# Kernel tuning notes

Hardware: AMD Instinct MI355X
Metric: run time of the kernel (lower is better)

The kernel has to match this reference:

```python
import jax, jax.numpy as jnp
import numpy as np

HEADS = 8

def setup_inputs() -> dict:
    key = jax.random.key(0)
    k1, k2, k3, k4 = jax.random.split(key, 4)
    B, C_IN, H, W = 16, 256, 64, 64
    C_OUT = 256
    s = 1.0 / np.sqrt(C_IN)
    x = jax.random.normal(k1, (B, C_IN, H, W), dtype=jnp.float32)
    wq = jax.random.normal(k2, (C_OUT, C_IN), dtype=jnp.float32) * s
    wk = jax.random.normal(k3, (C_OUT, C_IN), dtype=jnp.float32) * s
    wv = jax.random.normal(k4, (C_OUT, C_IN), dtype=jnp.float32) * s
    return {"x": x, "wq": wq, "wk": wk, "wv": wv}

def _feat(t):
    # ELU(x) + 1  (positive feature map for linear attention)
    return jax.nn.elu(t) + 1.0

def reference(x, wq, wk, wv):
    B, C, H, W = x.shape
    M = H * W
    c_out = wq.shape[0]
    dh = c_out // HEADS
    scale = 1.0 / np.sqrt(dh)
    xf = x.reshape(B, C, M)  # flatten spatial
    # 1x1 conv (no bias) == channel matmul; reshape to [B, heads, dh, M]
    def proj(w):
        return jnp.einsum('oc,bcm->bom', w, xf).reshape(B, HEADS, dh, M)
    q = _feat(proj(wq)) * scale
    k = _feat(proj(wk)) * scale
    v = proj(wv)
    # linear attention: KV = k v^T over spatial, then apply to q
    KV = jnp.einsum('bhcm,bhdm->bhcd', k, v)          # [B,h,dh,dh]
    out = jnp.einsum('bhcd,bhcm->bhdm', KV, q)        # [B,h,dh,M]
    k_sum = k.sum(axis=-1)                             # [B,h,dh]
    denom = jnp.einsum('bhcm,bhc->bhm', q, k_sum)      # [B,h,M]
    denom = jnp.maximum(denom, 1e-6)[:, :, None, :]
    out = out / denom
    return out.reshape(B, c_out, H, W)
```

## Files before the change

### kernel.cpp

```cpp
#include <hip/hip_runtime.h>
#include <hip/hip_bf16.h>


typedef __attribute__((ext_vector_type(8))) short bf16x8;
typedef __attribute__((ext_vector_type(4))) float f32x4;
typedef __attribute__((ext_vector_type(4))) unsigned int u32x4;
typedef __attribute__((ext_vector_type(4))) float float4v;

#define DEVI static __device__ __forceinline__

DEVI unsigned short f2bf(float f){
  unsigned int u = __builtin_bit_cast(unsigned int, f);
  u = (u + 0x7fffu + ((u >> 16) & 1u)) >> 16;
  return (unsigned short)u;
}
DEVI unsigned int pk2(float a, float b){
  return (unsigned int)f2bf(a) | ((unsigned int)f2bf(b) << 16);
}
DEVI float feat(float p){
  return (p > 0.f ? p + 1.f : __expf(p)) * 0.17677669529663687f;
}

DEVI f32x4 mfma16(u32x4 a, u32x4 b, f32x4 c){
  return __builtin_amdgcn_mfma_f32_16x16x32_bf16(
      __builtin_bit_cast(bf16x8, a), __builtin_bit_cast(bf16x8, b), c, 0, 0, 0);
}

DEVI int swz8(int m){ return ((m ^ (m >> 3)) & 7) << 4; }

typedef __attribute__((address_space(3))) unsigned int as3_u32;
typedef __attribute__((address_space(1))) const unsigned int as1_u32;
DEVI void gload16(const void* g, void* l){
  __builtin_amdgcn_global_load_lds((as1_u32*)g, (as3_u32*)l, 16, 0, 0);
}
DEVI void stage_tile(const char* src, void* buf, int w, int lane){
  #pragma unroll
  for (int i = 0; i < 4; ++i){
    int ub = w * 1024 + i * 8192;
    gload16(src + ub + lane * 16, (char*)buf + ub);
  }
}

DEVI void stage_load(const float* __restrict__ xb, int m0, int tid, float4v* r){
  #pragma unroll
  for (int it = 0; it < 2; ++it){
    int cq = (tid >> 4) + it * 32;
    int mq = tid & 15;
    const float* p = xb + (size_t)(cq * 4) * 4096 + m0 + mq * 4;
    r[it*4+0] = *(const float4v*)(p);
    r[it*4+1] = *(const float4v*)(p + 4096);
    r[it*4+2] = *(const float4v*)(p + 8192);
    r[it*4+3] = *(const float4v*)(p + 12288);
  }
}
DEVI void stage_write(unsigned short* xT, int tid, const float4v* r){
  #pragma unroll
  for (int it = 0; it < 2; ++it){
    int cq = (tid >> 4) + it * 32;
    int mq = tid & 15;
    int c0 = cq * 4, ml0 = mq * 4;
    #pragma unroll
    for (int j = 0; j < 4; ++j){
      int m = ml0 + j;
      unsigned int lo = pk2(r[it*4+0][j], r[it*4+1][j]);
      unsigned int hi = pk2(r[it*4+2][j], r[it*4+3][j]);
      int off = m * 512 + ((c0 * 2) ^ swz8(m));
      unsigned long long v = (unsigned long long)lo | ((unsigned long long)hi << 32);
      *(unsigned long long*)((char*)xT + off) = v;
    }
  }
}

DEVI void wpack(int t, const float* __restrict__ wq, const float* __restrict__ wk,
                const float* __restrict__ wv,
                unsigned short* __restrict__ wkvf, unsigned short* __restrict__ wqf){
  if (t < 16384){
    int lane = t & 63, kk = (t >> 6) & 7, ot = (t >> 9) & 3, h = t >> 11;
    int l15 = lane & 15, hi = lane >> 4;
    const float* src = (ot < 2) ? (wk + (size_t)(h * 32 + ot * 16 + l15) * 256)
                                : (wv + (size_t)(h * 32 + (ot - 2) * 16 + l15) * 256);
    src += kk * 32 + hi * 8;
    unsigned short* dst = wkvf + (size_t)t * 8;
    #pragma unroll
    for (int j = 0; j < 8; ++j) dst[j] = f2bf(src[j]);
  } else if (t < 24576){
    int u = t - 16384;
    int lane = u & 63, kk = (u >> 6) & 7, ot = (u >> 9) & 1, h = u >> 10;
    int l15 = lane & 15, hi = lane >> 4;
    const float* src = wq + (size_t)(h * 32 + ot * 16 + l15) * 256 + kk * 32 + hi * 8;
    unsigned short* dst = wqf + (size_t)u * 8;
    #pragma unroll
    for (int j = 0; j < 8; ++j) dst[j] = f2bf(src[j]);
  }
}

__global__ void __launch_bounds__(512) xcvt(const float* __restrict__ x,
        const float* __restrict__ wq, const float* __restrict__ wk,
        const float* __restrict__ wv,
        unsigned short* __restrict__ wkvf, unsigned short* __restrict__ wqf,
        unsigned short* __restrict__ ximg){
  __shared__ __align__(16) unsigned short xT[16384];
  const int tid = threadIdx.x;
  const int ch = blockIdx.x, b = blockIdx.y;
  if (ch >= 32){
    int t = ((ch - 32) * 16 + b) * 512 + tid;
    wpack(t, wq, wk, wv, wkvf, wqf);
    return;
  }
  const float* xb = x + (size_t)b * (256 * 4096);
  for (int sub = 0; sub < 2; ++sub){
    int m0 = ch * 128 + sub * 64;
    float4v rs[8];
    stage_load(xb, m0, tid, rs);
    if (sub) __syncthreads();
    stage_write(xT, tid, rs);
    __syncthreads();
    unsigned short* dst = ximg + ((size_t)b * 64 + (m0 >> 6)) * 16384;
    #pragma unroll
    for (int i = 0; i < 4; ++i){
      int f = i * 512 + tid;
      int lane = f & 63, nt = (f >> 6) & 3, kk = f >> 8;
      int m = nt * 16 + (lane & 15);
      int col = (kk * 64 + (lane >> 4) * 16) ^ swz8(m);
      u32x4 v = *(const u32x4*)((const char*)xT + m * 512 + col);
      *(u32x4*)((char*)dst + (size_t)f * 16) = v;
    }
  }
}

__global__ void __launch_bounds__(512) k_kv(const unsigned short* __restrict__ ximg,
        const unsigned short* __restrict__ wkvf,
        float* __restrict__ kvp, float* __restrict__ ksp){
  const int tid = threadIdx.x, lane = tid & 63, w = tid >> 6;
  const int l15 = lane & 15, hi = lane >> 4;
  const int ch = blockIdx.x, b = blockIdx.y;
  const unsigned short* tile = ximg + ((size_t)b * 64 + ch * 2) * 16384;

  f32x4 kvacc[2][2];
  f32x4 ksacc[2];
  #pragma unroll
  for (int i = 0; i < 2; ++i){
    ksacc[i] = f32x4{0.f,0.f,0.f,0.f};
    #pragma unroll
    for (int j = 0; j < 2; ++j) kvacc[i][j] = f32x4{0.f,0.f,0.f,0.f};
  }
  u32x4 ones = {0u,0u,0u,0u};
  if (l15 == 0){ ones[0] = ones[1] = ones[2] = ones[3] = 0x3f803f80u; }

  #pragma unroll
  for (int sub = 0; sub < 2; ++sub){
    const unsigned short* ts = tile + sub * 16384;
    #pragma unroll
    for (int g = 0; g < 2; ++g){
      f32x4 acc[2][4];
      #pragma unroll
      for (int a1 = 0; a1 < 2; ++a1)
        #pragma unroll
        for (int a2 = 0; a2 < 4; ++a2) acc[a1][a2] = f32x4{0.f,0.f,0.f,0.f};

      #pragma unroll
      for (int kk = 0; kk < 8; ++kk){
        u32x4 xf[2];
        #pragma unroll
        for (int n2 = 0; n2 < 2; ++n2){
          int nt = g * 2 + n2;
          xf[n2] = *(const u32x4*)(ts + (((size_t)kk * 4 + nt) * 64 + lane) * 8);
        }
        #pragma unroll
        for (int ot = 0; ot < 4; ++ot){
          u32x4 wf = *(const u32x4*)(wkvf + ((((size_t)w * 4 + ot) * 8 + kk) * 64 + lane) * 8);
          #pragma unroll
          for (int n2 = 0; n2 < 2; ++n2) acc[n2][ot] = mfma16(xf[n2], wf, acc[n2][ot]);
        }
      }
      u32x4 kf[2], vf[2];
      #pragma unroll
      for (int t2 = 0; t2 < 2; ++t2){
        kf[t2][0] = pk2(feat(acc[0][t2][0]), feat(acc[0][t2][1]));
        kf[t2][1] = pk2(feat(acc[0][t2][2]), feat(acc[0][t2][3]));
        kf[t2][2] = pk2(feat(acc[1][t2][0]), feat(acc[1][t2][1]));
        kf[t2][3] = pk2(feat(acc[1][t2][2]), feat(acc[1][t2][3]));
        vf[t2][0] = pk2(acc[0][t2+2][0], acc[0][t2+2][1]);
        vf[t2][1] = pk2(acc[0][t2+2][2], acc[0][t2+2][3]);
        vf[t2][2] = pk2(acc[1][t2+2][0], acc[1][t2+2][1]);
        vf[t2][3] = pk2(acc[1][t2+2][2], acc[1][t2+2][3]);
      }
      #pragma unroll
      for (int ct = 0; ct < 2; ++ct){
        #pragma unroll
        for (int dt = 0; dt < 2; ++dt)
          kvacc[ct][dt] = mfma16(kf[ct], vf[dt], kvacc[ct][dt]);
        ksacc[ct] = mfma16(kf[ct], ones, ksacc[ct]);
      }
    }
  }

  size_t base = (((size_t)b * 32 + ch) * 8 + w) * 1024;
  #pragma unroll
  for (int ct = 0; ct < 2; ++ct){
    #pragma unroll
    for (int dt = 0; dt < 2; ++dt){
      #pragma unroll
      for (int r = 0; r < 4; ++r){
        int c = ct * 16 + hi * 4 + r, d = dt * 16 + l15;
        kvp[base + c * 32 + d] = kvacc[ct][dt][r];
      }
    }
  }
  if (l15 == 0){
    size_t kb = (((size_t)b * 32 + ch) * 8 + w) * 32;
    #pragma unroll
    for (int ct = 0; ct < 2; ++ct)
      #pragma unroll
      for (int r = 0; r < 4; ++r) ksp[kb + ct * 16 + hi * 4 + r] = ksacc[ct][r];
  }
}

__global__ void k_red(const float* __restrict__ kvp, const float* __restrict__ ksp,
                      unsigned short* __restrict__ kvt, unsigned short* __restrict__ ksb){
  int t = blockIdx.x * 256 + threadIdx.x;
  int dq = t & 7;
  int c  = (t >> 3) & 31;
  int h  = (t >> 8) & 7;
  int b  = t >> 11;
  float4v s = {0.f,0.f,0.f,0.f};
  for (int c2 = 0; c2 < 32; ++c2){
    const float* p = kvp + ((((size_t)b * 32 + c2) * 8 + h) * 1024) + c * 32 + dq * 4;
    float4v r = *(const float4v*)p;
    s.x += r.x; s.y += r.y; s.z += r.z; s.w += r.w;
  }
  int pos = ((c >> 2) & 3) * 8 + ((c >> 4) << 2) + (c & 3);
  unsigned short* q = kvt + ((size_t)b * 8 + h) * 1024;
  q[(dq * 4 + 0) * 32 + pos] = f2bf(s.x);
  q[(dq * 4 + 1) * 32 + pos] = f2bf(s.y);
  q[(dq * 4 + 2) * 32 + pos] = f2bf(s.z);
  q[(dq * 4 + 3) * 32 + pos] = f2bf(s.w);
  if (dq == 0){
    float ks = 0.f;
    for (int c2 = 0; c2 < 32; ++c2)
      ks += ksp[(((size_t)b * 32 + c2) * 8 + h) * 32 + c];
    ksb[((size_t)b * 8 + h) * 32 + pos] = f2bf(ks);
  }
}

DEVI void q_sub(const unsigned short* __restrict__ xT,
                const unsigned short* __restrict__ wqf,
                u32x4 afkv0, u32x4 afkv1, u32x4 afd,
                int w, int l15, int hi, int lane, float* __restrict__ ob){
  f32x4 qa[2][4];
  #pragma unroll
  for (int a1 = 0; a1 < 2; ++a1)
    #pragma unroll
    for (int a2 = 0; a2 < 4; ++a2) qa[a1][a2] = f32x4{0.f,0.f,0.f,0.f};

  #pragma unroll
  for (int kk = 0; kk < 8; ++kk){
    u32x4 xf[4];
    #pragma unroll
    for (int nt = 0; nt < 4; ++nt)
      xf[nt] = *(const u32x4*)(xT + (((size_t)kk * 4 + nt) * 64 + lane) * 8);
    #pragma unroll
    for (int ot = 0; ot < 2; ++ot){
      u32x4 wf = *(const u32x4*)(wqf + ((((size_t)w * 2 + ot) * 8 + kk) * 64 + lane) * 8);
      #pragma unroll
      for (int nt = 0; nt < 4; ++nt) qa[ot][nt] = mfma16(wf, xf[nt], qa[ot][nt]);
    }
  }

  #pragma unroll
  for (int nt = 0; nt < 4; ++nt){
    u32x4 bq;
    bq[0] = pk2(feat(qa[0][nt][0]), feat(qa[0][nt][1]));
    bq[1] = pk2(feat(qa[0][nt][2]), feat(qa[0][nt][3]));
    bq[2] = pk2(feat(qa[1][nt][0]), feat(qa[1][nt][1]));
    bq[3] = pk2(feat(qa[1][nt][2]), feat(qa[1][nt][3]));

    f32x4 o0 = {0.f,0.f,0.f,0.f}, o1 = {0.f,0.f,0.f,0.f}, dn = {0.f,0.f,0.f,0.f};
    o0 = mfma16(afkv0, bq, o0);
    o1 = mfma16(afkv1, bq, o1);
    dn = mfma16(afd, bq, dn);
    float dv = __shfl(dn[0], l15, 64);
    float inv = 1.0f / fmaxf(dv, 1e-6f);
    #pragma unroll
    for (int r = 0; r < 4; ++r){
      ob[(size_t)(hi * 4 + r) * 4096 + nt * 16 + l15]      = o0[r] * inv;
      ob[(size_t)(16 + hi * 4 + r) * 4096 + nt * 16 + l15] = o1[r] * inv;
    }
  }
}

__global__ void __launch_bounds__(512) k_q(const unsigned short* __restrict__ ximg,
        const unsigned short* __restrict__ wqf,
        const unsigned short* __restrict__ kvt,
        const unsigned short* __restrict__ ksb,
        float* __restrict__ out){
  __shared__ __align__(16) unsigned short xT[2][16384];
  const int tid = threadIdx.x, lane = tid & 63, w = tid >> 6;
  const int l15 = lane & 15, hi = lane >> 4;
  const int ch = blockIdx.x, b = blockIdx.y;
  const char* src = (const char*)(ximg + ((size_t)b * 64 + ch * 2) * 16384);

  size_t kvbase = ((size_t)b * 8 + w) * 1024;
  u32x4 afkv0 = *(const u32x4*)(kvt + kvbase + (size_t)l15 * 32 + hi * 8);
  u32x4 afkv1 = *(const u32x4*)(kvt + kvbase + (size_t)(16 + l15) * 32 + hi * 8);
  u32x4 afd = {0u,0u,0u,0u};
  if (l15 == 0) afd = *(const u32x4*)(ksb + ((size_t)b * 8 + w) * 32 + hi * 8);

  stage_tile(src, xT[0], w, lane);
  __syncthreads();
  stage_tile(src + 32768, xT[1], w, lane);

  float* ob = out + ((size_t)b * 256 + w * 32) * 4096 + ch * 128;
  q_sub(xT[0], wqf, afkv0, afkv1, afd, w, l15, hi, lane, ob);
  __syncthreads();
  q_sub(xT[1], wqf, afkv0, afkv1, afd, w, l15, hi, lane, ob + 64);
}

extern "C" void kernel_launch(void* const* d_in, const int* in_sizes, int n_in,
                              void* d_out, int out_size, void* d_ws, size_t ws_size,
                              hipStream_t stream) {
  const float* x  = (const float*)d_in[0];
  const float* wq = (const float*)d_in[1];
  const float* wk = (const float*)d_in[2];
  const float* wv = (const float*)d_in[3];
  float* out = (float*)d_out;
  char* ws = (char*)d_ws;

  unsigned short* wkvf = (unsigned short*)(ws);
  unsigned short* wqf  = (unsigned short*)(ws + 262144);
  unsigned short* kvt  = (unsigned short*)(ws + 393216);
  unsigned short* ksb  = (unsigned short*)(ws + 655360);
  float* kvp = (float*)(ws + 1048576);
  float* ksp = (float*)(ws + 17825792);
  unsigned short* ximg = (unsigned short*)(ws + 18350080);

  hipLaunchKernelGGL(xcvt,  dim3(35, 16), dim3(512), 0, stream,
                     x, wq, wk, wv, wkvf, wqf, ximg);
  hipLaunchKernelGGL(k_kv,  dim3(32, 16), dim3(512), 0, stream, ximg, wkvf, kvp, ksp);
  hipLaunchKernelGGL(k_red, dim3(128), dim3(256), 0, stream, kvp, ksp, kvt, ksb);
  hipLaunchKernelGGL(k_q,   dim3(32, 16), dim3(512), 0, stream, ximg, wqf, kvt, ksb, out);
}
```

Baseline: 77.88 us.

## Fuse x bf16 conversion into KV kernel and split weight packing out

Weight packing moves into its own small kernel. The x fp32-to-bf16 transpose is merged into the KV projection kernel, which now computes K/V straight from swizzled shared memory while still writing the bf16 image for the Q kernel. The second sub-tile's global load is issued before the first sub-tile's compute, giving some overlap. This saves one pass of reading ximg back from global memory, at the cost of 64KB of LDS per block and the extra ximg write inside the compute kernel.

```diff
diff --git a/kernel.cpp b/kernel.cpp
--- a/kernel.cpp
+++ b/kernel.cpp
@@ -70,10 +70,22 @@
     }
   }
 }
-
-DEVI void wpack(int t, const float* __restrict__ wq, const float* __restrict__ wk,
-                const float* __restrict__ wv,
-                unsigned short* __restrict__ wkvf, unsigned short* __restrict__ wqf){
+DEVI void dump_tile_sw(const unsigned short* xT, unsigned short* dst, int tid){
+  #pragma unroll
+  for (int i = 0; i < 4; ++i){
+    int f = i * 512 + tid;
+    int lane = f & 63, nt = (f >> 6) & 3, kk = f >> 8;
+    int m = nt * 16 + (lane & 15);
+    int col = (kk * 64 + (lane >> 4) * 16) ^ swz8(m);
+    u32x4 v = *(const u32x4*)((const char*)xT + m * 512 + col);
+    *(u32x4*)((char*)dst + (size_t)f * 16) = v;
+  }
+}
+
+__global__ void wconv(const float* __restrict__ wq, const float* __restrict__ wk,
+                      const float* __restrict__ wv,
+                      unsigned short* __restrict__ wkvf, unsigned short* __restrict__ wqf){
+  int t = blockIdx.x * 256 + threadIdx.x;
   if (t < 16384){
     int lane = t & 63, kk = (t >> 6) & 7, ot = (t >> 9) & 3, h = t >> 11;
     int l15 = lane & 15, hi = lane >> 4;
@@ -94,47 +106,65 @@
   }
 }
 
-__global__ void __launch_bounds__(512) xcvt(const float* __restrict__ x,
-        const float* __restrict__ wq, const float* __restrict__ wk,
-        const float* __restrict__ wv,
-        unsigned short* __restrict__ wkvf, unsigned short* __restrict__ wqf,
-        unsigned short* __restrict__ ximg){
-  __shared__ __align__(16) unsigned short xT[16384];
-  const int tid = threadIdx.x;
-  const int ch = blockIdx.x, b = blockIdx.y;
-  if (ch >= 32){
-    int t = ((ch - 32) * 16 + b) * 512 + tid;
-    wpack(t, wq, wk, wv, wkvf, wqf);
-    return;
-  }
-  const float* xb = x + (size_t)b * (256 * 4096);
-  for (int sub = 0; sub < 2; ++sub){
-    int m0 = ch * 128 + sub * 64;
-    float4v rs[8];
-    stage_load(xb, m0, tid, rs);
-    if (sub) __syncthreads();
-    stage_write(xT, tid, rs);
-    __syncthreads();
-    unsigned short* dst = ximg + ((size_t)b * 64 + (m0 >> 6)) * 16384;
-    #pragma unroll
-    for (int i = 0; i < 4; ++i){
-      int f = i * 512 + tid;
-      int lane = f & 63, nt = (f >> 6) & 3, kk = f >> 8;
-      int m = nt * 16 + (lane & 15);
-      int col = (kk * 64 + (lane >> 4) * 16) ^ swz8(m);
-      u32x4 v = *(const u32x4*)((const char*)xT + m * 512 + col);
-      *(u32x4*)((char*)dst + (size_t)f * 16) = v;
-    }
-  }
-}
-
-__global__ void __launch_bounds__(512) k_kv(const unsigned short* __restrict__ ximg,
+DEVI void compute_sub_sw(const unsigned short* __restrict__ xT,
+                         const unsigned short* __restrict__ wkvf,
+                         int w, int l15, int hi, int lane,
+                         f32x4 (&kvacc)[2][2], f32x4 (&ksacc)[2], u32x4 ones){
+  #pragma unroll
+  for (int g = 0; g < 2; ++g){
+    f32x4 acc[2][4];
+    #pragma unroll
+    for (int a1 = 0; a1 < 2; ++a1)
+      #pragma unroll
+      for (int a2 = 0; a2 < 4; ++a2) acc[a1][a2] = f32x4{0.f,0.f,0.f,0.f};
+
+    #pragma unroll
+    for (int kk = 0; kk < 8; ++kk){
+      u32x4 xf[2];
+      #pragma unroll
+      for (int n2 = 0; n2 < 2; ++n2){
+        int m = (g * 2 + n2) * 16 + l15;
+        xf[n2] = *(const u32x4*)((const char*)xT + m * 512 + ((kk * 64 + hi * 16) ^ swz8(m)));
+      }
+      #pragma unroll
+      for (int ot = 0; ot < 4; ++ot){
+        u32x4 wf = *(const u32x4*)(wkvf + ((((size_t)w * 4 + ot) * 8 + kk) * 64 + lane) * 8);
+        #pragma unroll
+        for (int n2 = 0; n2 < 2; ++n2) acc[n2][ot] = mfma16(xf[n2], wf, acc[n2][ot]);
+      }
+    }
+    u32x4 kf[2], vf[2];
+    #pragma unroll
+    for (int t2 = 0; t2 < 2; ++t2){
+      kf[t2][0] = pk2(feat(acc[0][t2][0]), feat(acc[0][t2][1]));
+      kf[t2][1] = pk2(feat(acc[0][t2][2]), feat(acc[0][t2][3]));
+      kf[t2][2] = pk2(feat(acc[1][t2][0]), feat(acc[1][t2][1]));
+      kf[t2][3] = pk2(feat(acc[1][t2][2]), feat(acc[1][t2][3]));
+      vf[t2][0] = pk2(acc[0][t2+2][0], acc[0][t2+2][1]);
+      vf[t2][1] = pk2(acc[0][t2+2][2], acc[0][t2+2][3]);
+      vf[t2][2] = pk2(acc[1][t2+2][0], acc[1][t2+2][1]);
+      vf[t2][3] = pk2(acc[1][t2+2][2], acc[1][t2+2][3]);
+    }
+    #pragma unroll
+    for (int ct = 0; ct < 2; ++ct){
+      #pragma unroll
+      for (int dt = 0; dt < 2; ++dt)
+        kvacc[ct][dt] = mfma16(kf[ct], vf[dt], kvacc[ct][dt]);
+      ksacc[ct] = mfma16(kf[ct], ones, ksacc[ct]);
+    }
+  }
+}
+
+__global__ void __launch_bounds__(512) xkv(const float* __restrict__ x,
         const unsigned short* __restrict__ wkvf,
+        unsigned short* __restrict__ ximg,
         float* __restrict__ kvp, float* __restrict__ ksp){
+  __shared__ __align__(16) unsigned short xT[2][16384];
   const int tid = threadIdx.x, lane = tid & 63, w = tid >> 6;
   const int l15 = lane & 15, hi = lane >> 4;
   const int ch = blockIdx.x, b = blockIdx.y;
-  const unsigned short* tile = ximg + ((size_t)b * 64 + ch * 2) * 16384;
+  const float* xb = x + (size_t)b * (256 * 4096);
+  unsigned short* img = ximg + ((size_t)b * 64 + ch * 2) * 16384;
 
   f32x4 kvacc[2][2];
   f32x4 ksacc[2];
@@ -147,53 +177,17 @@
   u32x4 ones = {0u,0u,0u,0u};
   if (l15 == 0){ ones[0] = ones[1] = ones[2] = ones[3] = 0x3f803f80u; }
 
-  #pragma unroll
-  for (int sub = 0; sub < 2; ++sub){
-    const unsigned short* ts = tile + sub * 16384;
-    #pragma unroll
-    for (int g = 0; g < 2; ++g){
-      f32x4 acc[2][4];
-      #pragma unroll
-      for (int a1 = 0; a1 < 2; ++a1)
-        #pragma unroll
-        for (int a2 = 0; a2 < 4; ++a2) acc[a1][a2] = f32x4{0.f,0.f,0.f,0.f};
-
-      #pragma unroll
-      for (int kk = 0; kk < 8; ++kk){
-        u32x4 xf[2];
-        #pragma unroll
-        for (int n2 = 0; n2 < 2; ++n2){
-          int nt = g * 2 + n2;
-          xf[n2] = *(const u32x4*)(ts + (((size_t)kk * 4 + nt) * 64 + lane) * 8);
-        }
-        #pragma unroll
-        for (int ot = 0; ot < 4; ++ot){
-          u32x4 wf = *(const u32x4*)(wkvf + ((((size_t)w * 4 + ot) * 8 + kk) * 64 + lane) * 8);
-          #pragma unroll
-          for (int n2 = 0; n2 < 2; ++n2) acc[n2][ot] = mfma16(xf[n2], wf, acc[n2][ot]);
-        }
-      }
-      u32x4 kf[2], vf[2];
-      #pragma unroll
-      for (int t2 = 0; t2 < 2; ++t2){
-        kf[t2][0] = pk2(feat(acc[0][t2][0]), feat(acc[0][t2][1]));
-        kf[t2][1] = pk2(feat(acc[0][t2][2]), feat(acc[0][t2][3]));
-        kf[t2][2] = pk2(feat(acc[1][t2][0]), feat(acc[1][t2][1]));
-        kf[t2][3] = pk2(feat(acc[1][t2][2]), feat(acc[1][t2][3]));
-        vf[t2][0] = pk2(acc[0][t2+2][0], acc[0][t2+2][1]);
-        vf[t2][1] = pk2(acc[0][t2+2][2], acc[0][t2+2][3]);
-        vf[t2][2] = pk2(acc[1][t2+2][0], acc[1][t2+2][1]);
-        vf[t2][3] = pk2(acc[1][t2+2][2], acc[1][t2+2][3]);
-      }
-      #pragma unroll
-      for (int ct = 0; ct < 2; ++ct){
-        #pragma unroll
-        for (int dt = 0; dt < 2; ++dt)
-          kvacc[ct][dt] = mfma16(kf[ct], vf[dt], kvacc[ct][dt]);
-        ksacc[ct] = mfma16(kf[ct], ones, ksacc[ct]);
-      }
-    }
-  }
+  float4v rs[8];
+  stage_load(xb, ch * 128, tid, rs);
+  stage_write(xT[0], tid, rs);
+  __syncthreads();
+  stage_load(xb, ch * 128 + 64, tid, rs);
+  dump_tile_sw(xT[0], img, tid);
+  compute_sub_sw(xT[0], wkvf, w, l15, hi, lane, kvacc, ksacc, ones);
+  stage_write(xT[1], tid, rs);
+  __syncthreads();
+  dump_tile_sw(xT[1], img + 16384, tid);
+  compute_sub_sw(xT[1], wkvf, w, l15, hi, lane, kvacc, ksacc, ones);
 
   size_t base = (((size_t)b * 32 + ch) * 8 + w) * 1024;
   #pragma unroll
@@ -334,9 +328,8 @@
   float* ksp = (float*)(ws + 17825792);
   unsigned short* ximg = (unsigned short*)(ws + 18350080);
 
-  hipLaunchKernelGGL(xcvt,  dim3(35, 16), dim3(512), 0, stream,
-                     x, wq, wk, wv, wkvf, wqf, ximg);
-  hipLaunchKernelGGL(k_kv,  dim3(32, 16), dim3(512), 0, stream, ximg, wkvf, kvp, ksp);
+  hipLaunchKernelGGL(wconv, dim3(96), dim3(256), 0, stream, wq, wk, wv, wkvf, wqf);
+  hipLaunchKernelGGL(xkv,   dim3(32, 16), dim3(512), 0, stream, x, wkvf, ximg, kvp, ksp);
   hipLaunchKernelGGL(k_red, dim3(128), dim3(256), 0, stream, kvp, ksp, kvt, ksb);
   hipLaunchKernelGGL(k_q,   dim3(32, 16), dim3(512), 0, stream, ximg, wqf, kvt, ksb, out);
 }
```

Result: faster. 71.14 us (-8.7%).
